# Performance work log

Hardware: AMD Instinct MI355X
Metric: run time of the kernel (lower is better)

Reference implementation:

```python
import jax, jax.numpy as jnp
import numpy as np

K, T, F = 30000, 48, 4
EPS = 1e-5  # torch BatchNorm1d default eps


def _bn_params(key, c):
    k1, k2, k3, k4 = jax.random.split(key, 4)
    g = jax.random.uniform(k1, (c,), jnp.float32, 0.5, 1.5)
    b = jax.random.normal(k2, (c,), jnp.float32) * 0.1
    m = jax.random.normal(k3, (c,), jnp.float32) * 0.1
    v = jax.random.uniform(k4, (c,), jnp.float32, 0.5, 1.5)
    return g, b, m, v


def setup_inputs() -> dict:
    key = jax.random.key(0)
    ks = jax.random.split(key, 12)
    features = jax.random.normal(ks[0], (K, T, F), jnp.float32)
    # at least 1 valid point per non-empty voxel
    num_voxels = jnp.maximum(jax.random.randint(ks[1], (K,), 0, T), 1).astype(jnp.int32)
    coors = jax.random.randint(ks[2], (K, 3), 0, 100).astype(jnp.int32)
    # VFE1: in=8 (4 + 3 rel + 1 dist), units = 32//2 = 16
    w1 = jax.random.normal(ks[3], (8, 16), jnp.float32) / np.sqrt(8)
    b1 = jax.random.normal(ks[4], (16,), jnp.float32) * 0.01
    g1, be1, m1, v1 = _bn_params(ks[5], 16)
    # VFE2: in=32, units = 128//2 = 64
    w2 = jax.random.normal(ks[6], (32, 64), jnp.float32) / np.sqrt(32)
    b2 = jax.random.normal(ks[7], (64,), jnp.float32) * 0.01
    g2, be2, m2, v2 = _bn_params(ks[8], 64)
    # final linear 128 -> 128
    w3 = jax.random.normal(ks[9], (128, 128), jnp.float32) / np.sqrt(128)
    b3 = jax.random.normal(ks[10], (128,), jnp.float32) * 0.01
    g3, be3, m3, v3 = _bn_params(ks[11], 128)
    return dict(features=features, num_voxels=num_voxels, coors=coors,
                w1=w1, b1=b1, g1=g1, be1=be1, m1=m1, v1=v1,
                w2=w2, b2=b2, g2=g2, be2=be2, m2=m2, v2=v2,
                w3=w3, b3=b3, g3=g3, be3=be3, m3=m3, v3=v3)


def _bn(x, g, b, m, v):
    # eval-mode BatchNorm over last (channel) axis
    return (x - m) * (g / jnp.sqrt(v + EPS)) + b


def _vfe(x, W, b, g, be, m, v):
    # x: [K, T, Cin] -> [K, T, 2*units]
    h = jax.nn.relu(_bn(jnp.einsum('ktc,cu->ktu', x, W) + b, g, be, m, v))
    agg = jnp.max(h, axis=1, keepdims=True)  # [K, 1, U]
    return jnp.concatenate([h, jnp.broadcast_to(agg, h.shape)], axis=2)


def reference(features, num_voxels, coors,
              w1, b1, g1, be1, m1, v1,
              w2, b2, g2, be2, m2, v2,
              w3, b3, g3, be3, m3, v3):
    xyz = features[:, :, :3]
    nv = num_voxels.astype(features.dtype)[:, None, None]
    points_mean = jnp.sum(xyz, axis=1, keepdims=True) / nv
    rel = xyz - points_mean
    dist = jnp.linalg.norm(xyz, axis=2, keepdims=True)
    x = jnp.concatenate([features, rel, dist], axis=-1)  # [K, T, 8]
    mask = (jnp.arange(T)[None, :] < num_voxels[:, None]).astype(features.dtype)[:, :, None]
    x = x * mask
    x = _vfe(x, w1, b1, g1, be1, m1, v1) * mask   # [K, T, 32]
    x = _vfe(x, w2, b2, g2, be2, m2, v2) * mask   # [K, T, 128]
    x = jax.nn.relu(_bn(jnp.einsum('ktc,cu->ktu', x, w3) + b3, g3, be3, m3, v3)) * mask
    return jnp.max(x, axis=1)  # [K, 128]
```

## Files before the change

kernel.cpp:

```cpp
#include <hip/hip_runtime.h>

constexpr float EPS = 1e-5f;

typedef __attribute__((ext_vector_type(8))) short bf16x8;
typedef __attribute__((ext_vector_type(4))) float f32x4;

#define W2P_OFF 32768
#define W1P_OFF 40960
#define B1_OFF  41984
#define B2_OFF  42048
#define B3_OFF  42304

__device__ __forceinline__ ushort f2bf(float x) {
    union { float f; unsigned u; } a; a.f = x;
    unsigned r = a.u + 0x7fffu + ((a.u >> 16) & 1u);
    return (ushort)(r >> 16);
}

__device__ __forceinline__ unsigned cvtpk(float lo, float hi) {
    unsigned r;
    asm("v_cvt_pk_bf16_f32 %0, %1, %2" : "=v"(r) : "v"(lo), "v"(hi));
    return r;
}

__global__ void vfe_prep(
    const float* __restrict__ w1, const float* __restrict__ b1,
    const float* __restrict__ g1, const float* __restrict__ be1,
    const float* __restrict__ m1, const float* __restrict__ v1,
    const float* __restrict__ w2, const float* __restrict__ b2,
    const float* __restrict__ g2, const float* __restrict__ be2,
    const float* __restrict__ m2, const float* __restrict__ v2,
    const float* __restrict__ w3, const float* __restrict__ b3,
    const float* __restrict__ g3, const float* __restrict__ be3,
    const float* __restrict__ m3, const float* __restrict__ v3,
    void* __restrict__ ws)
{
    ushort* w3p = (ushort*)ws;
    ushort* w2p = (ushort*)((char*)ws + W2P_OFF);
    ushort* w1p = (ushort*)((char*)ws + W1P_OFF);
    float*  bb1 = (float*)((char*)ws + B1_OFF);
    float*  bb2 = (float*)((char*)ws + B2_OFF);
    float*  bb3 = (float*)((char*)ws + B3_OFF);

    const int i = blockIdx.x * 256 + threadIdx.x;
    if (i < 16384) {
        const int e = i & 7, l = (i >> 3) & 63, rest = i >> 9;
        const int ks = rest & 3, nt = rest >> 2, g = l >> 4;
        const int k = ks * 32 + g * 8 + e;
        const int n = nt * 16 + (l & 15);
        const float s = g3[n] * rsqrtf(v3[n] + EPS);
        w3p[i] = f2bf(w3[k * 128 + n] * s);
    } else if (i < 20480) {
        const int j = i - 16384;
        const int e = j & 7, l = (j >> 3) & 63, rest = j >> 9;
        const int nt = rest & 3, sel = rest >> 2;
        const int klog = (l >> 4) * 8 + e;
        const int n = nt * 16 + (l & 15);
        const float s = g2[n] * rsqrtf(v2[n] + EPS);
        w2p[j] = (klog < 16) ? f2bf(w2[(sel * 16 + klog) * 64 + n] * s) : (ushort)0;
    } else if (i < 20992) {
        const int j = i - 20480;
        const int e = j & 7, l = j >> 3;
        const int klog = (l >> 4) * 8 + e;
        const int u = l & 15;
        const float s = g1[u] * rsqrtf(v1[u] + EPS);
        w1p[j] = (klog < 8) ? f2bf(w1[klog * 16 + u] * s) : (ushort)0;
    } else if (i < 21200) {
        const int j = i - 20992;
        if (j < 16) {
            const int u = j;
            bb1[u] = (b1[u] - m1[u]) * (g1[u] * rsqrtf(v1[u] + EPS)) + be1[u];
        } else if (j < 80) {
            const int u = j - 16;
            bb2[u] = (b2[u] - m2[u]) * (g2[u] * rsqrtf(v2[u] + EPS)) + be2[u];
        } else {
            const int u = j - 80;
            bb3[u] = (b3[u] - m3[u]) * (g3[u] * rsqrtf(v3[u] + EPS)) + be3[u];
        }
    }
}

#define NV(v)   ((v)==0?nv0:(v)==1?nv1:(v)==2?nv2:nv3)
#define LIM(v)  ((v)==0?lim0:(v)==1?lim1:(v)==2?lim2:lim3)
#define FULL(v) ((v)==0?full0:(v)==1?full1:(v)==2?full2:full3)

__global__ __launch_bounds__(256, 4) void vfe_fused(
    const float* __restrict__ feat,
    const int* __restrict__ nvox,
    const void* __restrict__ ws,
    float* __restrict__ out,
    int K)
{
    __shared__ __align__(16) ushort sX0bf[192][8];
    __shared__ __align__(16) ushort sAfrag[12 * 16 * 24];
    __shared__ __align__(16) ushort sBfrag[12 * 2 * 64 * 8];
    __shared__ __align__(16) ushort sAgg1bf[4][16];
    __shared__ __align__(16) ushort sAgg2bf[4][64];

    const ushort* w3p = (const ushort*)ws;
    const ushort* w2p = (const ushort*)((const char*)ws + W2P_OFF);
    const ushort* w1p = (const ushort*)((const char*)ws + W1P_OFF);
    const float*  bb1 = (const float*)((const char*)ws + B1_OFF);
    const float*  bb2 = (const float*)((const char*)ws + B2_OFF);
    const float*  bb3 = (const float*)((const char*)ws + B3_OFF);

    const int tid  = threadIdx.x;
    const int lane = tid & 63;
    const int w    = tid >> 6;
    const int g    = lane >> 4;
    const int m15  = lane & 15;
    const int kA   = blockIdx.x * 4;

    int kk0 = kA, kk1 = min(kA+1, K-1), kk2 = min(kA+2, K-1), kk3 = min(kA+3, K-1);
    int nv0 = __builtin_amdgcn_readfirstlane(nvox[kk0]);
    int nv1 = __builtin_amdgcn_readfirstlane(nvox[kk1]);
    int nv2 = __builtin_amdgcn_readfirstlane(nvox[kk2]);
    int nv3 = __builtin_amdgcn_readfirstlane(nvox[kk3]);
    const int lim0=(nv0+15)>>4, lim1=(nv1+15)>>4, lim2=(nv2+15)>>4, lim3=(nv3+15)>>4;
    const int full0=nv0>>4, full1=nv1>>4, full2=nv2>>4, full3=nv3>>4;

    union U8 { bf16x8 v; unsigned u[4]; };

    const bf16x8 b1f   = *(const bf16x8*)(w1p + (size_t)lane * 8);
    const bf16x8 w2lof = *(const bf16x8*)(w2p + (size_t)((0 * 4 + w) * 64 + lane) * 8);
    const bf16x8 w2hif = *(const bf16x8*)(w2p + (size_t)((1 * 4 + w) * 64 + lane) * 8);
    bf16x8 b3f[2][4];
    #pragma unroll
    for (int nt = 0; nt < 2; ++nt)
        #pragma unroll
        for (int ks = 0; ks < 4; ++ks)
            b3f[nt][ks] = *(const bf16x8*)(w3p + (size_t)(((w * 2 + nt) * 4 + ks) * 64 + lane) * 8);

    {
        const int kkw = (w==0)?kk0:(w==1)?kk1:(w==2)?kk2:kk3;
        const int nvw = (w==0)?nv0:(w==1)?nv1:(w==2)?nv2:nv3;
        float4 f = make_float4(0.f, 0.f, 0.f, 0.f);
        if (lane < 48)
            f = *reinterpret_cast<const float4*>(feat + ((size_t)kkw * 48 + lane) * 4);
        float sx = f.x, sy = f.y, sz = f.z;
        #pragma unroll
        for (int d = 1; d < 64; d <<= 1) {
            sx += __shfl_xor(sx, d);
            sy += __shfl_xor(sy, d);
            sz += __shfl_xor(sz, d);
        }
        const float inv = 1.f / (float)nvw;
        if (lane < 48) {
            const float msk = (lane < nvw) ? 1.f : 0.f;
            const float dd = sqrtf(f.x * f.x + f.y * f.y + f.z * f.z);
            U8 a;
            a.u[0] = cvtpk(f.x * msk, f.y * msk);
            a.u[1] = cvtpk(f.z * msk, f.w * msk);
            a.u[2] = cvtpk((f.x - sx * inv) * msk, (f.y - sy * inv) * msk);
            a.u[3] = cvtpk((f.z - sz * inv) * msk, dd * msk);
            *reinterpret_cast<bf16x8*>(&sX0bf[w * 48 + lane][0]) = a.v;
        }
    }
    __syncthreads();

    {
        const float bb1u = bb1[m15];
        const int limw = (w==0)?lim0:(w==1)?lim1:(w==2)?lim2:lim3;
        float pmax = fmaxf(bb1u, 0.f);
        #pragma unroll
        for (int s = 0; s < 3; ++s) {
            if (s < limw) {
                const bf16x8 af = *(const bf16x8*)&sX0bf[w * 48 + s * 16 + m15][0];
                f32x4 ci = {bb1u, bb1u, bb1u, bb1u};
                f32x4 acc = __builtin_amdgcn_mfma_f32_16x16x32_bf16(af, b1f, ci, 0, 0, 0);
                #pragma unroll
                for (int r = 0; r < 4; ++r) {
                    const float h = fmaxf(acc[r], 0.f);
                    pmax = fmaxf(pmax, h);
                    sAfrag[((w * 3 + s) * 16 + g * 4 + r) * 24 + m15] = f2bf(h);
                }
            }
        }
        pmax = fmaxf(pmax, __shfl_xor(pmax, 16));
        pmax = fmaxf(pmax, __shfl_xor(pmax, 32));
        if (g == 0) sAgg1bf[w][m15] = f2bf(pmax);
    }
    __syncthreads();

    const int col2 = w * 16 + m15;
    const float bb2c = bb2[col2];
    f32x4 z2acc;
    {
        const bf16x8 az2 = *(const bf16x8*)&sAgg1bf[m15 & 3][(g & 1) * 8];
        f32x4 ci = {bb2c, bb2c, bb2c, bb2c};
        z2acc = __builtin_amdgcn_mfma_f32_16x16x32_bf16(az2, w2hif, ci, 0, 0, 0);
    }

    {
        const int ks = col2 >> 5, gp = (col2 >> 3) & 3, e = col2 & 7;
        #pragma unroll
        for (int vg = 0; vg < 2; ++vg) {
            f32x4 acc2[6];
            #pragma unroll
            for (int j = 0; j < 6; ++j) {
                const int tt = vg * 6 + j;
                const int vox = vg * 2 + j / 3;
                const int mtl = j % 3;
                if (mtl < LIM(vox)) {
                    const bf16x8 af = *(const bf16x8*)&sAfrag[(tt * 16 + m15) * 24 + (g & 1) * 8];
                    const float ci = z2acc[vox];
                    f32x4 c = {ci, ci, ci, ci};
                    acc2[j] = __builtin_amdgcn_mfma_f32_16x16x32_bf16(af, w2lof, c, 0, 0, 0);
                }
            }
            float mxP = fmaxf(bb2c, 0.f);
            float mxQ = fmaxf(bb2c, 0.f);
            #pragma unroll
            for (int j = 0; j < 6; ++j) {
                const int tt = vg * 6 + j;
                const int vox = vg * 2 + j / 3;
                const int mtl = j % 3;
                if (mtl < LIM(vox)) {
                    float h[4];
                    #pragma unroll
                    for (int r = 0; r < 4; ++r) {
                        h[r] = fmaxf(acc2[j][r], 0.f);
                        sBfrag[((tt * 2 + ks) * 64 + gp * 16 + (g * 4 + r)) * 8 + e] = f2bf(h[r]);
                    }
                    if (mtl < FULL(vox)) {
                        const float t01 = fmaxf(h[0], h[1]), t23 = fmaxf(h[2], h[3]);
                        if (j < 3) mxP = fmaxf(mxP, fmaxf(t01, t23));
                        else       mxQ = fmaxf(mxQ, fmaxf(t01, t23));
                    } else {
                        #pragma unroll
                        for (int r = 0; r < 4; ++r) {
                            if (mtl * 16 + g * 4 + r < NV(vox)) {
                                if (j < 3) mxP = fmaxf(mxP, h[r]);
                                else       mxQ = fmaxf(mxQ, h[r]);
                            }
                        }
                    }
                }
            }
            mxP = fmaxf(mxP, __shfl_xor(mxP, 16));
            mxP = fmaxf(mxP, __shfl_xor(mxP, 32));
            mxQ = fmaxf(mxQ, __shfl_xor(mxQ, 16));
            mxQ = fmaxf(mxQ, __shfl_xor(mxQ, 32));
            if (g == 0) {
                sAgg2bf[vg * 2 + 0][col2] = f2bf(mxP);
                sAgg2bf[vg * 2 + 1][col2] = f2bf(mxQ);
            }
        }
    }
    __syncthreads();

    f32x4 i3[2];
    #pragma unroll
    for (int nt = 0; nt < 2; ++nt) {
        const float bb3c = bb3[(w * 2 + nt) * 16 + m15];
        f32x4 z = {bb3c, bb3c, bb3c, bb3c};
        #pragma unroll
        for (int ks2 = 0; ks2 < 2; ++ks2) {
            const bf16x8 af = *(const bf16x8*)&sAgg2bf[m15 & 3][ks2 * 32 + g * 8];
            z = __builtin_amdgcn_mfma_f32_16x16x32_bf16(af, b3f[nt][2 + ks2], z, 0, 0, 0);
        }
        i3[nt] = z;
    }

    #pragma unroll
    for (int pass = 0; pass < 2; ++pass) {
        const int col = (w * 2 + pass) * 16 + m15;
        #pragma unroll
        for (int vg = 0; vg < 2; ++vg) {
            f32x4 acc3[6];
            #pragma unroll
            for (int j = 0; j < 6; ++j) {
                const int tt = vg * 6 + j;
                const int vox = vg * 2 + j / 3;
                const int mtl = j % 3;
                if (mtl < LIM(vox)) {
                    const bf16x8 af0 = *(const bf16x8*)&sBfrag[((tt * 2 + 0) * 64 + lane) * 8];
                    const bf16x8 af1 = *(const bf16x8*)&sBfrag[((tt * 2 + 1) * 64 + lane) * 8];
                    const float ci = i3[pass][vox];
                    f32x4 c = {ci, ci, ci, ci};
                    acc3[j] = __builtin_amdgcn_mfma_f32_16x16x32_bf16(af0, b3f[pass][0], c, 0, 0, 0);
                    acc3[j] = __builtin_amdgcn_mfma_f32_16x16x32_bf16(af1, b3f[pass][1], acc3[j], 0, 0, 0);
                }
            }
            float mxP = 0.f, mxQ = 0.f;
            #pragma unroll
            for (int j = 0; j < 6; ++j) {
                const int vox = vg * 2 + j / 3;
                const int mtl = j % 3;
                if (mtl < FULL(vox)) {
                    const float t01 = fmaxf(acc3[j][0], acc3[j][1]);
                    const float t23 = fmaxf(acc3[j][2], acc3[j][3]);
                    if (j < 3) mxP = fmaxf(mxP, fmaxf(t01, t23));
                    else       mxQ = fmaxf(mxQ, fmaxf(t01, t23));
                } else if (mtl < LIM(vox)) {
                    #pragma unroll
                    for (int r = 0; r < 4; ++r) {
                        if (mtl * 16 + g * 4 + r < NV(vox)) {
                            if (j < 3) mxP = fmaxf(mxP, acc3[j][r]);
                            else       mxQ = fmaxf(mxQ, acc3[j][r]);
                        }
                    }
                }
            }
            mxP = fmaxf(mxP, __shfl_xor(mxP, 16));
            mxP = fmaxf(mxP, __shfl_xor(mxP, 32));
            mxQ = fmaxf(mxQ, __shfl_xor(mxQ, 16));
            mxQ = fmaxf(mxQ, __shfl_xor(mxQ, 32));
            if (g == (vg * 2 + 0) && (kA + vg * 2 + 0) < K) out[(size_t)(kA + vg * 2 + 0) * 128 + col] = mxP;
            if (g == (vg * 2 + 1) && (kA + vg * 2 + 1) < K) out[(size_t)(kA + vg * 2 + 1) * 128 + col] = mxQ;
        }
    }
}

extern "C" void kernel_launch(void* const* d_in, const int* in_sizes, int n_in,
                              void* d_out, int out_size, void* d_ws, size_t ws_size,
                              hipStream_t stream) {
    const float* feat = (const float*)d_in[0];
    const int*   nvx  = (const int*)d_in[1];
    const float* w1 = (const float*)d_in[3];
    const float* b1 = (const float*)d_in[4];
    const float* g1 = (const float*)d_in[5];
    const float* be1= (const float*)d_in[6];
    const float* m1 = (const float*)d_in[7];
    const float* v1 = (const float*)d_in[8];
    const float* w2 = (const float*)d_in[9];
    const float* b2 = (const float*)d_in[10];
    const float* g2 = (const float*)d_in[11];
    const float* be2= (const float*)d_in[12];
    const float* m2 = (const float*)d_in[13];
    const float* v2 = (const float*)d_in[14];
    const float* w3 = (const float*)d_in[15];
    const float* b3 = (const float*)d_in[16];
    const float* g3 = (const float*)d_in[17];
    const float* be3= (const float*)d_in[18];
    const float* m3 = (const float*)d_in[19];
    const float* v3 = (const float*)d_in[20];
    float* out = (float*)d_out;

    const int K = in_sizes[1];

    vfe_prep<<<84, 256, 0, stream>>>(w1,b1,g1,be1,m1,v1, w2,b2,g2,be2,m2,v2,
                                     w3,b3,g3,be3,m3,v3, d_ws);
    vfe_fused<<<(K + 3) / 4, 256, 0, stream>>>(feat, nvx, d_ws, out, K);
}
```

Baseline: 73.97 us.

## Make each wave own one voxel for VFE1/VFE2 using transposed MFMAs

Restructures the first two layers so each wave processes its own voxel end to end. The MFMA operands are swapped (weights as A, points as B) and weights are repacked into a transposed layout, so the per-voxel max reduces within a wave via shuffles. This removes two block-wide barriers and the shared agg1 buffer. The VFE2 output goes to an XOR-swizzled shared layout to reduce bank conflicts, the input staging reuses that shared buffer, and W3 fragment loads move after the barrier to shorten live ranges. The trade-off is more shuffle work per wave and more register pressure from the four-column accumulators.

```diff
diff --git a/kernel.cpp b/kernel.cpp
--- a/kernel.cpp
+++ b/kernel.cpp
@@ -5,11 +5,12 @@
 typedef __attribute__((ext_vector_type(8))) short bf16x8;
 typedef __attribute__((ext_vector_type(4))) float f32x4;
 
-#define W2P_OFF 32768
-#define W1P_OFF 40960
-#define B1_OFF  41984
-#define B2_OFF  42048
-#define B3_OFF  42304
+#define W2TL_OFF 32768
+#define W2TH_OFF 36864
+#define W1T_OFF  40960
+#define B1_OFF   41984
+#define B2_OFF   42048
+#define B3_OFF   42304
 
 __device__ __forceinline__ ushort f2bf(float x) {
     union { float f; unsigned u; } a; a.f = x;
@@ -20,6 +21,20 @@
 __device__ __forceinline__ unsigned cvtpk(float lo, float hi) {
     unsigned r;
     asm("v_cvt_pk_bf16_f32 %0, %1, %2" : "=v"(r) : "v"(lo), "v"(hi));
+    return r;
+}
+
+__device__ __forceinline__ f32x4 vmax4(f32x4 a, f32x4 b) {
+    f32x4 r;
+    r[0] = fmaxf(a[0], b[0]); r[1] = fmaxf(a[1], b[1]);
+    r[2] = fmaxf(a[2], b[2]); r[3] = fmaxf(a[3], b[3]);
+    return r;
+}
+
+__device__ __forceinline__ f32x4 shflx4(f32x4 v, int m) {
+    f32x4 r;
+    r[0] = __shfl_xor(v[0], m); r[1] = __shfl_xor(v[1], m);
+    r[2] = __shfl_xor(v[2], m); r[3] = __shfl_xor(v[3], m);
     return r;
 }
 
@@ -35,12 +50,13 @@
     const float* __restrict__ m3, const float* __restrict__ v3,
     void* __restrict__ ws)
 {
-    ushort* w3p = (ushort*)ws;
-    ushort* w2p = (ushort*)((char*)ws + W2P_OFF);
-    ushort* w1p = (ushort*)((char*)ws + W1P_OFF);
-    float*  bb1 = (float*)((char*)ws + B1_OFF);
-    float*  bb2 = (float*)((char*)ws + B2_OFF);
-    float*  bb3 = (float*)((char*)ws + B3_OFF);
+    ushort* w3p  = (ushort*)ws;
+    ushort* w2tl = (ushort*)((char*)ws + W2TL_OFF);
+    ushort* w2th = (ushort*)((char*)ws + W2TH_OFF);
+    ushort* w1t  = (ushort*)((char*)ws + W1T_OFF);
+    float*  bb1  = (float*)((char*)ws + B1_OFF);
+    float*  bb2  = (float*)((char*)ws + B2_OFF);
+    float*  bb3  = (float*)((char*)ws + B3_OFF);
 
     const int i = blockIdx.x * 256 + threadIdx.x;
     if (i < 16384) {
@@ -50,21 +66,27 @@
         const int n = nt * 16 + (l & 15);
         const float s = g3[n] * rsqrtf(v3[n] + EPS);
         w3p[i] = f2bf(w3[k * 128 + n] * s);
+    } else if (i < 18432) {
+        const int j = i - 16384;
+        const int e = j & 7, l = (j >> 3) & 63, mc = j >> 9;
+        const int slot = (l >> 4) * 8 + e;
+        const int m = mc * 16 + (l & 15);
+        const float s = g2[m] * rsqrtf(v2[m] + EPS);
+        w2tl[j] = (slot < 16) ? f2bf(w2[slot * 64 + m] * s) : (ushort)0;
     } else if (i < 20480) {
-        const int j = i - 16384;
-        const int e = j & 7, l = (j >> 3) & 63, rest = j >> 9;
-        const int nt = rest & 3, sel = rest >> 2;
-        const int klog = (l >> 4) * 8 + e;
-        const int n = nt * 16 + (l & 15);
-        const float s = g2[n] * rsqrtf(v2[n] + EPS);
-        w2p[j] = (klog < 16) ? f2bf(w2[(sel * 16 + klog) * 64 + n] * s) : (ushort)0;
+        const int j = i - 18432;
+        const int e = j & 7, l = (j >> 3) & 63, mc = j >> 9;
+        const int slot = (l >> 4) * 8 + e;
+        const int m = mc * 16 + (l & 15);
+        const float s = g2[m] * rsqrtf(v2[m] + EPS);
+        w2th[j] = (slot < 16) ? f2bf(w2[(16 + slot) * 64 + m] * s) : (ushort)0;
     } else if (i < 20992) {
         const int j = i - 20480;
         const int e = j & 7, l = j >> 3;
-        const int klog = (l >> 4) * 8 + e;
-        const int u = l & 15;
-        const float s = g1[u] * rsqrtf(v1[u] + EPS);
-        w1p[j] = (klog < 8) ? f2bf(w1[klog * 16 + u] * s) : (ushort)0;
+        const int slot = (l >> 4) * 8 + e;
+        const int m = l & 15;
+        const float s = g1[m] * rsqrtf(v1[m] + EPS);
+        w1t[j] = (slot < 8) ? f2bf(w1[slot * 16 + m] * s) : (ushort)0;
     } else if (i < 21200) {
         const int j = i - 20992;
         if (j < 16) {
@@ -91,18 +113,17 @@
     float* __restrict__ out,
     int K)
 {
-    __shared__ __align__(16) ushort sX0bf[192][8];
-    __shared__ __align__(16) ushort sAfrag[12 * 16 * 24];
-    __shared__ __align__(16) ushort sBfrag[12 * 2 * 64 * 8];
-    __shared__ __align__(16) ushort sAgg1bf[4][16];
-    __shared__ __align__(16) ushort sAgg2bf[4][64];
-
-    const ushort* w3p = (const ushort*)ws;
-    const ushort* w2p = (const ushort*)((const char*)ws + W2P_OFF);
-    const ushort* w1p = (const ushort*)((const char*)ws + W1P_OFF);
-    const float*  bb1 = (const float*)((const char*)ws + B1_OFF);
-    const float*  bb2 = (const float*)((const char*)ws + B2_OFF);
-    const float*  bb3 = (const float*)((const char*)ws + B3_OFF);
+    __shared__ __align__(16) ushort sBfrag[12 * 16 * 64];
+    __shared__ __align__(16) ushort sAfrag[12 * 16 * 16];
+    __shared__ __align__(16) ushort sAgg2bf[4 * 64];
+
+    const ushort* w3p  = (const ushort*)ws;
+    const ushort* w2tl = (const ushort*)((const char*)ws + W2TL_OFF);
+    const ushort* w2th = (const ushort*)((const char*)ws + W2TH_OFF);
+    const ushort* w1t  = (const ushort*)((const char*)ws + W1T_OFF);
+    const float*  bb1  = (const float*)((const char*)ws + B1_OFF);
+    const float*  bb2  = (const float*)((const char*)ws + B2_OFF);
+    const float*  bb3  = (const float*)((const char*)ws + B3_OFF);
 
     const int tid  = threadIdx.x;
     const int lane = tid & 63;
@@ -111,29 +132,23 @@
     const int m15  = lane & 15;
     const int kA   = blockIdx.x * 4;
 
-    int kk0 = kA, kk1 = min(kA+1, K-1), kk2 = min(kA+2, K-1), kk3 = min(kA+3, K-1);
-    int nv0 = __builtin_amdgcn_readfirstlane(nvox[kk0]);
-    int nv1 = __builtin_amdgcn_readfirstlane(nvox[kk1]);
-    int nv2 = __builtin_amdgcn_readfirstlane(nvox[kk2]);
-    int nv3 = __builtin_amdgcn_readfirstlane(nvox[kk3]);
+    const int kk0 = kA, kk1 = min(kA+1, K-1), kk2 = min(kA+2, K-1), kk3 = min(kA+3, K-1);
+    const int nv0 = __builtin_amdgcn_readfirstlane(nvox[kk0]);
+    const int nv1 = __builtin_amdgcn_readfirstlane(nvox[kk1]);
+    const int nv2 = __builtin_amdgcn_readfirstlane(nvox[kk2]);
+    const int nv3 = __builtin_amdgcn_readfirstlane(nvox[kk3]);
     const int lim0=(nv0+15)>>4, lim1=(nv1+15)>>4, lim2=(nv2+15)>>4, lim3=(nv3+15)>>4;
     const int full0=nv0>>4, full1=nv1>>4, full2=nv2>>4, full3=nv3>>4;
 
+    const int kkw   = (w==0)?kk0:(w==1)?kk1:(w==2)?kk2:kk3;
+    const int nvw   = (w==0)?nv0:(w==1)?nv1:(w==2)?nv2:nv3;
+    const int limw  = (nvw + 15) >> 4;
+    const int fullw = nvw >> 4;
+
     union U8 { bf16x8 v; unsigned u[4]; };
 
-    const bf16x8 b1f   = *(const bf16x8*)(w1p + (size_t)lane * 8);
-    const bf16x8 w2lof = *(const bf16x8*)(w2p + (size_t)((0 * 4 + w) * 64 + lane) * 8);
-    const bf16x8 w2hif = *(const bf16x8*)(w2p + (size_t)((1 * 4 + w) * 64 + lane) * 8);
-    bf16x8 b3f[2][4];
-    #pragma unroll
-    for (int nt = 0; nt < 2; ++nt)
-        #pragma unroll
-        for (int ks = 0; ks < 4; ++ks)
-            b3f[nt][ks] = *(const bf16x8*)(w3p + (size_t)(((w * 2 + nt) * 4 + ks) * 64 + lane) * 8);
-
+    ushort* sX0w = &sBfrag[w * 3 * 1024];
     {
-        const int kkw = (w==0)?kk0:(w==1)?kk1:(w==2)?kk2:kk3;
-        const int nvw = (w==0)?nv0:(w==1)?nv1:(w==2)?nv2:nv3;
         float4 f = make_float4(0.f, 0.f, 0.f, 0.f);
         if (lane < 48)
             f = *reinterpret_cast<const float4*>(feat + ((size_t)kkw * 48 + lane) * 4);
@@ -153,101 +168,104 @@
             a.u[1] = cvtpk(f.z * msk, f.w * msk);
             a.u[2] = cvtpk((f.x - sx * inv) * msk, (f.y - sy * inv) * msk);
             a.u[3] = cvtpk((f.z - sz * inv) * msk, dd * msk);
-            *reinterpret_cast<bf16x8*>(&sX0bf[w * 48 + lane][0]) = a.v;
-        }
-    }
-    __syncthreads();
-
+            *reinterpret_cast<bf16x8*>(sX0w + (size_t)lane * 8) = a.v;
+        }
+    }
+
+    const bf16x8 w1f = *(const bf16x8*)(w1t + (size_t)lane * 8);
+    const f32x4 bb1v = *(const f32x4*)(bb1 + g * 4);
+    f32x4 agg1 = vmax4(bb1v, (f32x4){0.f,0.f,0.f,0.f});
+    #pragma unroll
+    for (int nt = 0; nt < 3; ++nt) {
+        if (nt < limw) {
+            const bf16x8 x0b = *(const bf16x8*)(sX0w + (size_t)(nt * 16 + m15) * 8);
+            f32x4 acc = __builtin_amdgcn_mfma_f32_16x16x32_bf16(w1f, x0b, bb1v, 0, 0, 0);
+            f32x4 h = vmax4(acc, (f32x4){0.f,0.f,0.f,0.f});
+            agg1 = vmax4(agg1, h);
+            *reinterpret_cast<uint2*>(sAfrag + (size_t)(w * 3 + nt) * 256 + m15 * 16 + g * 4) =
+                make_uint2(cvtpk(h[0], h[1]), cvtpk(h[2], h[3]));
+        }
+    }
+    #pragma unroll
+    for (int s = 1; s < 16; s <<= 1) agg1 = vmax4(agg1, shflx4(agg1, s));
+
+    f32x4 z2acc[4];
+    f32x4 bb2v[4];
     {
-        const float bb1u = bb1[m15];
-        const int limw = (w==0)?lim0:(w==1)?lim1:(w==2)?lim2:lim3;
-        float pmax = fmaxf(bb1u, 0.f);
-        #pragma unroll
-        for (int s = 0; s < 3; ++s) {
-            if (s < limw) {
-                const bf16x8 af = *(const bf16x8*)&sX0bf[w * 48 + s * 16 + m15][0];
-                f32x4 ci = {bb1u, bb1u, bb1u, bb1u};
-                f32x4 acc = __builtin_amdgcn_mfma_f32_16x16x32_bf16(af, b1f, ci, 0, 0, 0);
+        const int src0 = ((g * 2)     & 3) * 16 + m15;
+        const int src1 = ((g * 2 + 1) & 3) * 16 + m15;
+        const float a0 = __shfl(agg1[0], src0), a1 = __shfl(agg1[1], src0);
+        const float a2 = __shfl(agg1[2], src0), a3 = __shfl(agg1[3], src0);
+        const float c0 = __shfl(agg1[0], src1), c1 = __shfl(agg1[1], src1);
+        const float c2 = __shfl(agg1[2], src1), c3 = __shfl(agg1[3], src1);
+        U8 az2;
+        az2.u[0] = cvtpk(a0, a1); az2.u[1] = cvtpk(a2, a3);
+        az2.u[2] = cvtpk(c0, c1); az2.u[3] = cvtpk(c2, c3);
+        #pragma unroll
+        for (int mc = 0; mc < 4; ++mc) {
+            bb2v[mc] = *(const f32x4*)(bb2 + mc * 16 + g * 4);
+            const bf16x8 whi = *(const bf16x8*)(w2th + (size_t)(mc * 64 + lane) * 8);
+            z2acc[mc] = __builtin_amdgcn_mfma_f32_16x16x32_bf16(whi, az2.v, bb2v[mc], 0, 0, 0);
+        }
+    }
+
+    f32x4 agg2acc[4];
+    #pragma unroll
+    for (int mc = 0; mc < 4; ++mc) agg2acc[mc] = vmax4(bb2v[mc], (f32x4){0.f,0.f,0.f,0.f});
+    {
+        bf16x8 wlo[4];
+        #pragma unroll
+        for (int mc = 0; mc < 4; ++mc)
+            wlo[mc] = *(const bf16x8*)(w2tl + (size_t)(mc * 64 + lane) * 8);
+        const int swz = (m15 & 7) << 4;
+        #pragma unroll
+        for (int nt = 0; nt < 3; ++nt) {
+            if (nt < limw) {
+                const bf16x8 xb = *(const bf16x8*)(sAfrag + (size_t)(w * 3 + nt) * 256 + m15 * 16 + (g & 1) * 8);
+                f32x4 h[4];
                 #pragma unroll
-                for (int r = 0; r < 4; ++r) {
-                    const float h = fmaxf(acc[r], 0.f);
-                    pmax = fmaxf(pmax, h);
-                    sAfrag[((w * 3 + s) * 16 + g * 4 + r) * 24 + m15] = f2bf(h);
+                for (int mc = 0; mc < 4; ++mc) {
+                    f32x4 acc = __builtin_amdgcn_mfma_f32_16x16x32_bf16(wlo[mc], xb, z2acc[mc], 0, 0, 0);
+                    h[mc] = vmax4(acc, (f32x4){0.f,0.f,0.f,0.f});
                 }
-            }
-        }
-        pmax = fmaxf(pmax, __shfl_xor(pmax, 16));
-        pmax = fmaxf(pmax, __shfl_xor(pmax, 32));
-        if (g == 0) sAgg1bf[w][m15] = f2bf(pmax);
-    }
-    __syncthreads();
-
-    const int col2 = w * 16 + m15;
-    const float bb2c = bb2[col2];
-    f32x4 z2acc;
-    {
-        const bf16x8 az2 = *(const bf16x8*)&sAgg1bf[m15 & 3][(g & 1) * 8];
-        f32x4 ci = {bb2c, bb2c, bb2c, bb2c};
-        z2acc = __builtin_amdgcn_mfma_f32_16x16x32_bf16(az2, w2hif, ci, 0, 0, 0);
-    }
-
-    {
-        const int ks = col2 >> 5, gp = (col2 >> 3) & 3, e = col2 & 7;
-        #pragma unroll
-        for (int vg = 0; vg < 2; ++vg) {
-            f32x4 acc2[6];
-            #pragma unroll
-            for (int j = 0; j < 6; ++j) {
-                const int tt = vg * 6 + j;
-                const int vox = vg * 2 + j / 3;
-                const int mtl = j % 3;
-                if (mtl < LIM(vox)) {
-                    const bf16x8 af = *(const bf16x8*)&sAfrag[(tt * 16 + m15) * 24 + (g & 1) * 8];
-                    const float ci = z2acc[vox];
-                    f32x4 c = {ci, ci, ci, ci};
-                    acc2[j] = __builtin_amdgcn_mfma_f32_16x16x32_bf16(af, w2lof, c, 0, 0, 0);
-                }
-            }
-            float mxP = fmaxf(bb2c, 0.f);
-            float mxQ = fmaxf(bb2c, 0.f);
-            #pragma unroll
-            for (int j = 0; j < 6; ++j) {
-                const int tt = vg * 6 + j;
-                const int vox = vg * 2 + j / 3;
-                const int mtl = j % 3;
-                if (mtl < LIM(vox)) {
-                    float h[4];
+                if (nt < fullw) {
                     #pragma unroll
-                    for (int r = 0; r < 4; ++r) {
-                        h[r] = fmaxf(acc2[j][r], 0.f);
-                        sBfrag[((tt * 2 + ks) * 64 + gp * 16 + (g * 4 + r)) * 8 + e] = f2bf(h[r]);
-                    }
-                    if (mtl < FULL(vox)) {
-                        const float t01 = fmaxf(h[0], h[1]), t23 = fmaxf(h[2], h[3]);
-                        if (j < 3) mxP = fmaxf(mxP, fmaxf(t01, t23));
-                        else       mxQ = fmaxf(mxQ, fmaxf(t01, t23));
-                    } else {
+                    for (int mc = 0; mc < 4; ++mc) agg2acc[mc] = vmax4(agg2acc[mc], h[mc]);
+                } else {
+                    const bool p = (nt * 16 + m15) < nvw;
+                    #pragma unroll
+                    for (int mc = 0; mc < 4; ++mc) {
                         #pragma unroll
-                        for (int r = 0; r < 4; ++r) {
-                            if (mtl * 16 + g * 4 + r < NV(vox)) {
-                                if (j < 3) mxP = fmaxf(mxP, h[r]);
-                                else       mxQ = fmaxf(mxQ, h[r]);
-                            }
-                        }
+                        for (int r = 0; r < 4; ++r)
+                            agg2acc[mc][r] = p ? fmaxf(agg2acc[mc][r], h[mc][r]) : agg2acc[mc][r];
                     }
                 }
+                char* rowp = (char*)sBfrag + (size_t)(w * 3 + nt) * 2048 + m15 * 128;
+                #pragma unroll
+                for (int mc = 0; mc < 4; ++mc)
+                    *reinterpret_cast<uint2*>(rowp + ((mc * 32 + g * 8) ^ swz)) =
+                        make_uint2(cvtpk(h[mc][0], h[mc][1]), cvtpk(h[mc][2], h[mc][3]));
             }
-            mxP = fmaxf(mxP, __shfl_xor(mxP, 16));
-            mxP = fmaxf(mxP, __shfl_xor(mxP, 32));
-            mxQ = fmaxf(mxQ, __shfl_xor(mxQ, 16));
-            mxQ = fmaxf(mxQ, __shfl_xor(mxQ, 32));
-            if (g == 0) {
-                sAgg2bf[vg * 2 + 0][col2] = f2bf(mxP);
-                sAgg2bf[vg * 2 + 1][col2] = f2bf(mxQ);
-            }
-        }
+        }
+    }
+    #pragma unroll
+    for (int s = 1; s < 16; s <<= 1) {
+        #pragma unroll
+        for (int mc = 0; mc < 4; ++mc) agg2acc[mc] = vmax4(agg2acc[mc], shflx4(agg2acc[mc], s));
+    }
+    if (m15 < 4) {
+        const f32x4 v = (m15==0)?agg2acc[0]:(m15==1)?agg2acc[1]:(m15==2)?agg2acc[2]:agg2acc[3];
+        *reinterpret_cast<uint2*>((char*)sAgg2bf + w * 128 + m15 * 32 + g * 8) =
+            make_uint2(cvtpk(v[0], v[1]), cvtpk(v[2], v[3]));
     }
     __syncthreads();
+
+    bf16x8 b3f[2][4];
+    #pragma unroll
+    for (int nt = 0; nt < 2; ++nt)
+        #pragma unroll
+        for (int ks = 0; ks < 4; ++ks)
+            b3f[nt][ks] = *(const bf16x8*)(w3p + (size_t)(((w * 2 + nt) * 4 + ks) * 64 + lane) * 8);
 
     f32x4 i3[2];
     #pragma unroll
@@ -256,12 +274,13 @@
         f32x4 z = {bb3c, bb3c, bb3c, bb3c};
         #pragma unroll
         for (int ks2 = 0; ks2 < 2; ++ks2) {
-            const bf16x8 af = *(const bf16x8*)&sAgg2bf[m15 & 3][ks2 * 32 + g * 8];
+            const bf16x8 af = *(const bf16x8*)(sAgg2bf + (size_t)(m15 & 3) * 64 + ks2 * 32 + g * 8);
             z = __builtin_amdgcn_mfma_f32_16x16x32_bf16(af, b3f[nt][2 + ks2], z, 0, 0, 0);
         }
         i3[nt] = z;
     }
 
+    const int swzr = (m15 & 7) << 4;
     #pragma unroll
     for (int pass = 0; pass < 2; ++pass) {
         const int col = (w * 2 + pass) * 16 + m15;
@@ -274,8 +293,9 @@
                 const int vox = vg * 2 + j / 3;
                 const int mtl = j % 3;
                 if (mtl < LIM(vox)) {
-                    const bf16x8 af0 = *(const bf16x8*)&sBfrag[((tt * 2 + 0) * 64 + lane) * 8];
-                    const bf16x8 af1 = *(const bf16x8*)&sBfrag[((tt * 2 + 1) * 64 + lane) * 8];
+                    const char* base = (const char*)sBfrag + (size_t)tt * 2048 + m15 * 128;
+                    const bf16x8 af0 = *(const bf16x8*)(base + ((g * 16) ^ swzr));
+                    const bf16x8 af1 = *(const bf16x8*)(base + ((64 + g * 16) ^ swzr));
                     const float ci = i3[pass][vox];
                     f32x4 c = {ci, ci, ci, ci};
                     acc3[j] = __builtin_amdgcn_mfma_f32_16x16x32_bf16(af0, b3f[pass][0], c, 0, 0, 0);
```

Measured after the change: 83.77 us. +13.2%, slower.
